# Optimization experiments

Hardware: AMD Instinct MI355X
Metric: run time of the kernel (lower is better)

The kernel has to match this reference:

```python
import jax, jax.numpy as jnp
import numpy as np

N_TOK, BATCH, D, MEM, H, W = 196, 64, 256, 2048, 16, 16


def setup_inputs() -> dict:
    key = jax.random.key(0)
    ks = jax.random.split(key, 9)
    w_scale = 1.0 / np.sqrt(D)  # ~ Linear default init scale
    return {
        "input_tokens": jax.random.normal(ks[0], (N_TOK, BATCH, D), jnp.float32),
        "ch_memory": jax.random.normal(ks[1], (MEM, D), jnp.float32) * 0.1,
        "ch_wq": jax.random.normal(ks[2], (D, D), jnp.float32) * w_scale,
        "ch_wk": jax.random.normal(ks[3], (D, D), jnp.float32) * w_scale,
        "ch_wv": jax.random.normal(ks[4], (D, D), jnp.float32) * w_scale,
        "sp_memory": jax.random.normal(ks[5], (MEM, H, W), jnp.float32) * 0.1,
        "sp_wq": jax.random.normal(ks[6], (D, D), jnp.float32) * w_scale,
        "sp_wk": jax.random.normal(ks[7], (D, D), jnp.float32) * w_scale,
        "sp_wv": jax.random.normal(ks[8], (D, D), jnp.float32) * w_scale,
    }


def reference(input_tokens, ch_memory, ch_wq, ch_wk, ch_wv,
              sp_memory, sp_wq, sp_wk, sp_wv):
    n_tok, batch, d = input_tokens.shape
    hw = d  # spatial branch requires feature_dim == H*W
    x = input_tokens.reshape(n_tok * batch, d)  # [NB, D]

    # ---- Channel memory branch: dot-product softmax read ----
    q = x @ ch_wq.T                       # [NB, D]
    k = ch_memory @ ch_wk.T               # [M, D]
    v = ch_memory @ ch_wv.T               # [M, D]
    scores = (q @ k.T) * (1.0 / jnp.sqrt(jnp.float32(d)))  # [NB, M]
    att_c = jax.nn.softmax(scores, axis=-1)
    out_c = att_c @ v                     # [NB, D]

    # ---- Spatial memory branch: SSIM-score softmax read ----
    mem_flat = sp_memory.reshape(sp_memory.shape[0], hw)  # [M, HW]
    qf = x @ sp_wq.T                      # [NB, HW]
    kf = mem_flat @ sp_wk.T               # [M, HW]
    vf = mem_flat @ sp_wv.T               # [M, HW]

    q_mean = jnp.mean(qf, axis=1, keepdims=True)          # [NB, 1]
    k_mean = jnp.mean(kf, axis=1, keepdims=True)          # [M, 1]
    q_var = jnp.var(qf, axis=1, ddof=1, keepdims=True)    # unbiased, like torch.var
    k_var = jnp.var(kf, axis=1, ddof=1, keepdims=True)
    cov = ((qf - q_mean) @ (kf - k_mean).T) / jnp.float32(hw - 1)  # [NB, M]

    c1, c2 = 0.01, 0.03
    mean_prod = q_mean @ k_mean.T                          # [NB, M]
    numerator = (2.0 * mean_prod + c1) * (2.0 * cov + c2)
    denominator = (q_mean ** 2 + (k_mean.T) ** 2 + c1) * (q_var + k_var.T + c2)
    ssim = numerator / (denominator + 1e-8)                # [NB, M]

    att_s = jax.nn.softmax(ssim, axis=-1)
    out_s = att_s @ vf                     # [NB, HW] == [NB, D]

    return (out_c + out_s).reshape(n_tok, batch, d)
```

## Files before the change

### kernel.cpp

```cpp
#include <hip/hip_runtime.h>

#define NBQ 12544
#define DM  256
#define MM  2048

typedef __attribute__((ext_vector_type(8)))  __bf16 bf16x8;
typedef __attribute__((ext_vector_type(4)))  float  floatx4;

__device__ __forceinline__ ushort f2bf(float x) {
    unsigned u = __float_as_uint(x);
    u += 0x7fffu + ((u >> 16) & 1u);
    return (ushort)(u >> 16);
}
__device__ __forceinline__ float bf2f(ushort h) {
    return __uint_as_float(((unsigned)h) << 16);
}
__device__ __forceinline__ ushort4 cvt4(float4 f) {
    union { __bf16 h[4]; ushort4 u; } r;
    r.h[0] = (__bf16)f.x; r.h[1] = (__bf16)f.y;
    r.h[2] = (__bf16)f.z; r.h[3] = (__bf16)f.w;
    return r.u;
}

__device__ __forceinline__ void glds16(const ushort* g, ushort* l) {
    __builtin_amdgcn_global_load_lds(
        (const __attribute__((address_space(1))) unsigned int*)g,
        (__attribute__((address_space(3))) unsigned int*)l, 16, 0, 0);
}

__global__ __launch_bounds__(256) void cvt_all_bf16(
    const float* __restrict__ x,   const float* __restrict__ ch_mem,
    const float* __restrict__ sp_mem,
    const float* __restrict__ cwq, const float* __restrict__ swq,
    const float* __restrict__ cwk, const float* __restrict__ cwv,
    const float* __restrict__ swk, const float* __restrict__ swv,
    ushort* __restrict__ xb, ushort* __restrict__ cmb,
    ushort* __restrict__ smb, ushort* __restrict__ wb)
{
    int bid = blockIdx.x;
    const float* src; ushort* dst; size_t off;
    if (bid < 392)      { src = x;      dst = xb;  off = (size_t)bid * 8192; }
    else if (bid < 456) { src = ch_mem; dst = cmb; off = (size_t)(bid - 392) * 8192; }
    else if (bid < 520) { src = sp_mem; dst = smb; off = (size_t)(bid - 456) * 8192; }
    else {
        int w = bid - 520, wi = w >> 3;
        if      (wi == 0) src = cwq;
        else if (wi == 1) src = swq;
        else if (wi == 2) src = cwk;
        else if (wi == 3) src = cwv;
        else if (wi == 4) src = swk;
        else              src = swv;
        dst = wb + (size_t)wi * 65536;
        off = (size_t)(w & 7) * 8192;
    }
    #pragma unroll
    for (int i = 0; i < 4; ++i) {
        size_t b = off + (size_t)i * 2048 + (size_t)threadIdx.x * 8;
        float4 a0 = *(const float4*)(src + b);
        float4 a1 = *(const float4*)(src + b + 4);
        *(ushort4*)(dst + b)     = cvt4(a0);
        *(ushort4*)(dst + b + 4) = cvt4(a1);
    }
}

#define PSTG(b, d0_)                                                          \
    { _Pragma("unroll") for (int p = 0; p < 2; ++p) {                         \
        int j = wv * 2 + p;                                                   \
        int R = j * 8 + (lane >> 3);                                          \
        int so = R * 256 + (d0_) + (((lane & 7) ^ (R & 7)) << 3);             \
        int doff = j * 512;                                                   \
        glds16(As_ + so, &SM[b][0][0][0] + doff);                             \
        glds16(W1_ + so, &SM[b][1][0][0] + doff);                             \
        glds16(W2_ + so, &SM[b][2][0][0] + doff);                             \
    } }

__global__ __launch_bounds__(256, 3) void gemm_proj_bf16(
    const ushort* __restrict__ xb,  const ushort* __restrict__ cmb,
    const ushort* __restrict__ smb, const ushort* __restrict__ wb,
    ushort* __restrict__ Qb,  ushort* __restrict__ QFb,
    ushort* __restrict__ Kb,  ushort* __restrict__ KFb,
    ushort* __restrict__ Vtb, ushort* __restrict__ VFtb)
{
    __shared__ ushort SM[2][3][64][64];

    int bid = blockIdx.x;
    const ushort* A; const ushort* W1; const ushort* W2;
    ushort* C1; ushort* C2; int nrows, trans2;
    if (bid < 784) {
        A = xb; W1 = wb; W2 = wb + 65536; C1 = Qb; C2 = QFb; nrows = NBQ; trans2 = 0;
    } else if (bid < 912) {
        A = cmb; W1 = wb + 2 * 65536; W2 = wb + 3 * 65536; C1 = Kb; C2 = Vtb;
        nrows = MM; trans2 = 1; bid -= 784;
    } else {
        A = smb; W1 = wb + 4 * 65536; W2 = wb + 5 * 65536; C1 = KFb; C2 = VFtb;
        nrows = MM; trans2 = 1; bid -= 912;
    }
    const int r0 = (bid >> 2) * 64;
    const int c0 = (bid & 3) * 64;

    const int tid  = threadIdx.x;
    const int wv   = tid >> 6;
    const int lane = tid & 63;
    const int quad = lane >> 4;
    const int l16  = lane & 15;
    const int rw = (wv & 1) * 32;
    const int cw = (wv >> 1) * 32;

    const ushort* As_ = A  + (size_t)r0 * 256;
    const ushort* W1_ = W1 + (size_t)c0 * 256;
    const ushort* W2_ = W2 + (size_t)c0 * 256;

    floatx4 acc1[2][2], acc2[2][2];
    #pragma unroll
    for (int i = 0; i < 2; ++i)
        #pragma unroll
        for (int j = 0; j < 2; ++j) {
            acc1[i][j] = (floatx4){0.f, 0.f, 0.f, 0.f};
            acc2[i][j] = (floatx4){0.f, 0.f, 0.f, 0.f};
        }

    PSTG(0, 0);
    __syncthreads();

    int buf = 0;
    const int kx = l16 & 7;
    for (int d0 = 0; d0 < 256; d0 += 64) {
        if (d0 + 64 < 256) PSTG(buf ^ 1, d0 + 64);
        #pragma unroll
        for (int kk = 0; kk < 64; kk += 32) {
            int off = (((kk >> 3) + quad) ^ kx) << 3;
            bf16x8 aA0 = *(const bf16x8*)&SM[buf][0][rw + l16][off];
            bf16x8 aA1 = *(const bf16x8*)&SM[buf][0][rw + 16 + l16][off];
            bf16x8 b10 = *(const bf16x8*)&SM[buf][1][cw + l16][off];
            bf16x8 b11 = *(const bf16x8*)&SM[buf][1][cw + 16 + l16][off];
            bf16x8 b20 = *(const bf16x8*)&SM[buf][2][cw + l16][off];
            bf16x8 b21 = *(const bf16x8*)&SM[buf][2][cw + 16 + l16][off];
            acc1[0][0] = __builtin_amdgcn_mfma_f32_16x16x32_bf16(aA0, b10, acc1[0][0], 0, 0, 0);
            acc1[0][1] = __builtin_amdgcn_mfma_f32_16x16x32_bf16(aA0, b11, acc1[0][1], 0, 0, 0);
            acc1[1][0] = __builtin_amdgcn_mfma_f32_16x16x32_bf16(aA1, b10, acc1[1][0], 0, 0, 0);
            acc1[1][1] = __builtin_amdgcn_mfma_f32_16x16x32_bf16(aA1, b11, acc1[1][1], 0, 0, 0);
            acc2[0][0] = __builtin_amdgcn_mfma_f32_16x16x32_bf16(aA0, b20, acc2[0][0], 0, 0, 0);
            acc2[0][1] = __builtin_amdgcn_mfma_f32_16x16x32_bf16(aA0, b21, acc2[0][1], 0, 0, 0);
            acc2[1][0] = __builtin_amdgcn_mfma_f32_16x16x32_bf16(aA1, b20, acc2[1][0], 0, 0, 0);
            acc2[1][1] = __builtin_amdgcn_mfma_f32_16x16x32_bf16(aA1, b21, acc2[1][1], 0, 0, 0);
        }
        __syncthreads();
        buf ^= 1;
    }

    #pragma unroll
    for (int ag = 0; ag < 2; ++ag)
        #pragma unroll
        for (int cg = 0; cg < 2; ++cg)
            #pragma unroll
            for (int i = 0; i < 4; ++i)
                C1[(size_t)(r0 + rw + ag * 16 + quad * 4 + i) * 256
                   + c0 + cw + cg * 16 + l16] = f2bf(acc1[ag][cg][i]);

    if (!trans2) {
        #pragma unroll
        for (int ag = 0; ag < 2; ++ag)
            #pragma unroll
            for (int cg = 0; cg < 2; ++cg)
                #pragma unroll
                for (int i = 0; i < 4; ++i)
                    C2[(size_t)(r0 + rw + ag * 16 + quad * 4 + i) * 256
                       + c0 + cw + cg * 16 + l16] = f2bf(acc2[ag][cg][i]);
    } else {
        __syncthreads();
        ushort (*W2s)[64] = SM[0][2];
        #pragma unroll
        for (int ag = 0; ag < 2; ++ag)
            #pragma unroll
            for (int cg = 0; cg < 2; ++cg)
                #pragma unroll
                for (int i = 0; i < 4; ++i) {
                    int col = rw + ag * 16 + quad * 4 + i;
                    int R   = cw + cg * 16 + l16;
                    W2s[R][(((col >> 3) ^ (R & 7)) << 3) + (col & 7)] =
                        f2bf(acc2[ag][cg][i]);
                }
        __syncthreads();
        const int col = tid >> 2;
        const int cj0 = (tid & 3) * 2;
        #pragma unroll
        for (int j = 0; j < 2; ++j) {
            int oc = cj0 + j;
            *(uint4*)(C2 + (size_t)(c0 + col) * nrows + r0 + oc * 8) =
                *(const uint4*)&W2s[col][(oc ^ (col & 7)) << 3];
        }
    }
}

__global__ __launch_bounds__(256) void gemm_proj_all(
    const float* __restrict__ x,      const float* __restrict__ ch_mem,
    const float* __restrict__ ch_wq,  const float* __restrict__ ch_wk,
    const float* __restrict__ ch_wv,  const float* __restrict__ sp_mem,
    const float* __restrict__ sp_wq,  const float* __restrict__ sp_wk,
    const float* __restrict__ sp_wv,
    ushort* __restrict__ Qb,  ushort* __restrict__ QFb,
    ushort* __restrict__ Kb,  ushort* __restrict__ KFb,
    ushort* __restrict__ Vtb, ushort* __restrict__ VFtb)
{
    __shared__ ushort As[64][72];
    __shared__ ushort W1s[64][72];
    __shared__ ushort W2s[64][72];

    int bid = blockIdx.x;
    const float* A; const float* W1; const float* W2;
    ushort* C1; ushort* C2; int nrows, trans2;
    if (bid < 784) {
        A = x; W1 = ch_wq; W2 = sp_wq; C1 = Qb; C2 = QFb; nrows = NBQ; trans2 = 0;
    } else if (bid < 912) {
        A = ch_mem; W1 = ch_wk; W2 = ch_wv; C1 = Kb; C2 = Vtb;
        nrows = MM; trans2 = 1; bid -= 784;
    } else {
        A = sp_mem; W1 = sp_wk; W2 = sp_wv; C1 = KFb; C2 = VFtb;
        nrows = MM; trans2 = 1; bid -= 912;
    }
    const int r0 = (bid >> 2) * 64;
    const int c0 = (bid & 3) * 64;

    const int tid  = threadIdx.x;
    const int wv   = tid >> 6;
    const int lane = tid & 63;
    const int quad = lane >> 4;
    const int l16  = lane & 15;
    const int rw = (wv & 1) * 32;
    const int cw = (wv >> 1) * 32;

    floatx4 acc1[2][2], acc2[2][2];
    #pragma unroll
    for (int i = 0; i < 2; ++i)
        #pragma unroll
        for (int j = 0; j < 2; ++j) {
            acc1[i][j] = (floatx4){0.f, 0.f, 0.f, 0.f};
            acc2[i][j] = (floatx4){0.f, 0.f, 0.f, 0.f};
        }

    float4 a4[4], w14[4], w24[4];
    #pragma unroll
    for (int it = 0; it < 4; ++it) {
        int idx = tid + it * 256;
        int r = idx >> 4, c4 = (idx & 15) * 4;
        a4[it]  = *(const float4*)(A  + (size_t)(r0 + r) * 256 + c4);
        w14[it] = *(const float4*)(W1 + (size_t)(c0 + r) * 256 + c4);
        w24[it] = *(const float4*)(W2 + (size_t)(c0 + r) * 256 + c4);
    }

    for (int d0 = 0; d0 < 256; d0 += 64) {
        __syncthreads();
        #pragma unroll
        for (int it = 0; it < 4; ++it) {
            int idx = tid + it * 256;
            int r = idx >> 4, c4 = (idx & 15) * 4;
            *(ushort4*)&As[r][c4]  = cvt4(a4[it]);
            *(ushort4*)&W1s[r][c4] = cvt4(w14[it]);
            *(ushort4*)&W2s[r][c4] = cvt4(w24[it]);
        }
        if (d0 + 64 < 256) {
            #pragma unroll
            for (int it = 0; it < 4; ++it) {
                int idx = tid + it * 256;
                int r = idx >> 4, c4 = (idx & 15) * 4;
                a4[it]  = *(const float4*)(A  + (size_t)(r0 + r) * 256 + d0 + 64 + c4);
                w14[it] = *(const float4*)(W1 + (size_t)(c0 + r) * 256 + d0 + 64 + c4);
                w24[it] = *(const float4*)(W2 + (size_t)(c0 + r) * 256 + d0 + 64 + c4);
            }
        }
        __syncthreads();
        #pragma unroll
        for (int kk = 0; kk < 64; kk += 32) {
            bf16x8 aA0 = *(const bf16x8*)&As[rw + l16][kk + quad * 8];
            bf16x8 aA1 = *(const bf16x8*)&As[rw + 16 + l16][kk + quad * 8];
            bf16x8 b10 = *(const bf16x8*)&W1s[cw + l16][kk + quad * 8];
            bf16x8 b11 = *(const bf16x8*)&W1s[cw + 16 + l16][kk + quad * 8];
            bf16x8 b20 = *(const bf16x8*)&W2s[cw + l16][kk + quad * 8];
            bf16x8 b21 = *(const bf16x8*)&W2s[cw + 16 + l16][kk + quad * 8];
            acc1[0][0] = __builtin_amdgcn_mfma_f32_16x16x32_bf16(aA0, b10, acc1[0][0], 0, 0, 0);
            acc1[0][1] = __builtin_amdgcn_mfma_f32_16x16x32_bf16(aA0, b11, acc1[0][1], 0, 0, 0);
            acc1[1][0] = __builtin_amdgcn_mfma_f32_16x16x32_bf16(aA1, b10, acc1[1][0], 0, 0, 0);
            acc1[1][1] = __builtin_amdgcn_mfma_f32_16x16x32_bf16(aA1, b11, acc1[1][1], 0, 0, 0);
            acc2[0][0] = __builtin_amdgcn_mfma_f32_16x16x32_bf16(aA0, b20, acc2[0][0], 0, 0, 0);
            acc2[0][1] = __builtin_amdgcn_mfma_f32_16x16x32_bf16(aA0, b21, acc2[0][1], 0, 0, 0);
            acc2[1][0] = __builtin_amdgcn_mfma_f32_16x16x32_bf16(aA1, b20, acc2[1][0], 0, 0, 0);
            acc2[1][1] = __builtin_amdgcn_mfma_f32_16x16x32_bf16(aA1, b21, acc2[1][1], 0, 0, 0);
        }
    }

    #pragma unroll
    for (int ag = 0; ag < 2; ++ag)
        #pragma unroll
        for (int cg = 0; cg < 2; ++cg)
            #pragma unroll
            for (int i = 0; i < 4; ++i)
                C1[(size_t)(r0 + rw + ag * 16 + quad * 4 + i) * 256
                   + c0 + cw + cg * 16 + l16] = f2bf(acc1[ag][cg][i]);

    if (!trans2) {
        #pragma unroll
        for (int ag = 0; ag < 2; ++ag)
            #pragma unroll
            for (int cg = 0; cg < 2; ++cg)
                #pragma unroll
                for (int i = 0; i < 4; ++i)
                    C2[(size_t)(r0 + rw + ag * 16 + quad * 4 + i) * 256
                       + c0 + cw + cg * 16 + l16] = f2bf(acc2[ag][cg][i]);
    } else {
        __syncthreads();
        #pragma unroll
        for (int ag = 0; ag < 2; ++ag)
            #pragma unroll
            for (int cg = 0; cg < 2; ++cg)
                #pragma unroll
                for (int i = 0; i < 4; ++i)
                    W2s[cw + cg * 16 + l16][rw + ag * 16 + quad * 4 + i] = f2bf(acc2[ag][cg][i]);
        __syncthreads();
        const int col = tid >> 2;
        const int seg = (tid & 3) * 16;
        #pragma unroll
        for (int j = 0; j < 2; ++j)
            *(uint4*)(C2 + (size_t)(c0 + col) * nrows + r0 + seg + j * 8) =
                *(const uint4*)&W2s[col][seg + j * 8];
    }
}

__global__ __launch_bounds__(256) void row_stats_kf(
    const ushort* __restrict__ KFb, float* __restrict__ km, float* __restrict__ kv)
{
    const int row  = blockIdx.x * 4 + (threadIdx.x >> 6);
    const int lane = threadIdx.x & 63;
    ushort4 u = *(const ushort4*)(KFb + (size_t)row * 256 + lane * 4);
    float a = bf2f(u.x), b = bf2f(u.y), c = bf2f(u.z), d = bf2f(u.w);
    float s  = a + b + c + d;
    float ss = a * a + b * b + c * c + d * d;
    #pragma unroll
    for (int off = 32; off > 0; off >>= 1) {
        s  += __shfl_down(s, off);
        ss += __shfl_down(ss, off);
    }
    if (lane == 0) {
        float m = s * (1.f / 256.f);
        km[row] = m;
        kv[row] = (ss - 256.f * m * m) * (1.f / 255.f) + 0.03f;
    }
}

#define STAGE_TILE(b, ti)                                                     \
    {                                                                         \
        const ushort* kp_ = kp0 + (size_t)(ti) * 32 * DM;                     \
        const ushort* vp_ = vp0 + (ti) * 32;                                  \
        ushort* dst_ = SMu + (b) * 16384;                                     \
        _Pragma("unroll")                                                     \
        for (int p = 0; p < 4; ++p) {                                         \
            int db = (wv * 4 + p) * 512;                                      \
            glds16(kp_ + offK[p], dst_ + db);                                 \
            glds16(vp_ + offV[p], dst_ + 8192 + db);                          \
        }                                                                     \
    }

template<int NHALF>
__global__ __launch_bounds__(256, 2) void fused_attn_1br(
    const ushort* __restrict__ Qb,  const ushort* __restrict__ QFb,
    const ushort* __restrict__ Kb,  const ushort* __restrict__ KFb,
    const ushort* __restrict__ Vtb, const ushort* __restrict__ VFtb,
    const float* __restrict__ km_, const float* __restrict__ kv_,
    float* __restrict__ part, float* __restrict__ denp)
{
    __shared__ ushort SMu[32768];

    const int tid  = threadIdx.x;
    const int wv   = tid >> 6;
    const int lane = tid & 63;
    const int quad = lane >> 4;
    const int l16  = lane & 15;

    const int NQC = NBQ / 128;
    const int per_br = NQC * NHALF;
    int bid = blockIdx.x;
    const int br  = (bid < per_br) ? 1 : 0;
    int rem = br ? bid : bid - per_br;
    const int half = rem / NQC;
    const int qc   = rem - half * NQC;
    const int q0   = qc * 128;
    const int kbase = half * (MM / NHALF);
    const int NT   = (MM / NHALF) / 32;

    const ushort* qsrc = br ? QFb : Qb;
    const ushort* Ksel = br ? KFb : Kb;
    const ushort* Vsel = br ? VFtb : Vtb;

    bf16x8 aQ0[8], aQ1[8];
    {
        const ushort* qp = qsrc + (size_t)(q0 + wv * 32 + l16) * DM + quad * 8;
        #pragma unroll
        for (int s = 0; s < 8; ++s) {
            aQ0[s] = *(const bf16x8*)(qp + s * 32);
            aQ1[s] = *(const bf16x8*)(qp + 16 * DM + s * 32);
        }
    }

    float qmv0 = 0.f, qvv0 = 0.f, qmv1 = 0.f, qvv1 = 0.f, qm20 = 0.f, qm21 = 0.f;
    if (br) {
        float s0 = 0.f, ss0 = 0.f, s1 = 0.f, ss1 = 0.f;
        #pragma unroll
        for (int s = 0; s < 8; ++s)
            #pragma unroll
            for (int j = 0; j < 8; ++j) {
                float v0 = (float)aQ0[s][j], v1 = (float)aQ1[s][j];
                s0 += v0; ss0 += v0 * v0; s1 += v1; ss1 += v1 * v1;
            }
        s0  += __shfl_xor(s0, 16, 64);  s0  += __shfl_xor(s0, 32, 64);
        ss0 += __shfl_xor(ss0, 16, 64); ss0 += __shfl_xor(ss0, 32, 64);
        s1  += __shfl_xor(s1, 16, 64);  s1  += __shfl_xor(s1, 32, 64);
        ss1 += __shfl_xor(ss1, 16, 64); ss1 += __shfl_xor(ss1, 32, 64);
        qmv0 = s0 * (1.f / 256.f);
        qvv0 = (ss0 - 256.f * qmv0 * qmv0) * (1.f / 255.f);
        qmv1 = s1 * (1.f / 256.f);
        qvv1 = (ss1 - 256.f * qmv1 * qmv1) * (1.f / 255.f);
        qm20 = qmv0 * qmv0 + 0.01f;
        qm21 = qmv1 * qmv1 + 0.01f;
    }

    int offK[4], offV[4];
    #pragma unroll
    for (int p = 0; p < 4; ++p) {
        int j  = wv * 4 + p;
        int Rk = 2 * j + (lane >> 5);
        int rk = (Rk & 3) + ((Rk >> 4) & 1) * 4 + ((Rk >> 2) & 3) * 8;
        int ck = (lane & 31) ^ (Rk & 7);
        offK[p] = rk * DM + ck * 8;
        int Rv = 16 * j + (lane >> 2);
        int cv = (lane & 3) ^ (Rv & 3);
        offV[p] = Rv * MM + cv * 8;
    }

    const ushort* kp0 = Ksel + (size_t)kbase * DM;
    const ushort* vp0 = Vsel + kbase;

    floatx4 acc0[16], acc1[16];
    #pragma unroll
    for (int t = 0; t < 16; ++t) {
        acc0[t] = (floatx4){0.f, 0.f, 0.f, 0.f};
        acc1[t] = (floatx4){0.f, 0.f, 0.f, 0.f};
    }
    float den0 = 0.f, den1 = 0.f;
    const int ksw  = l16 & 7;
    const int vswo = (quad ^ (l16 & 3)) * 8;

    STAGE_TILE(0, 0);
    __syncthreads();

    int buf = 0;
    for (int ti = 0; ti < NT; ++ti) {
        if (ti + 1 < NT) STAGE_TILE(buf ^ 1, ti + 1);

        const ushort* Ks = SMu + buf * 16384;
        const ushort* Vs = Ks + 8192;

        floatx4 S00 = (floatx4){0.f, 0.f, 0.f, 0.f};
        floatx4 S10 = (floatx4){0.f, 0.f, 0.f, 0.f};
        floatx4 S01 = (floatx4){0.f, 0.f, 0.f, 0.f};
        floatx4 S11 = (floatx4){0.f, 0.f, 0.f, 0.f};
        #pragma unroll
        for (int s = 0; s < 8; ++s) {
            int off = ((s * 4 + quad) ^ ksw) * 8;
            bf16x8 aK0 = *(const bf16x8*)(Ks + l16 * DM + off);
            bf16x8 aK1 = *(const bf16x8*)(Ks + 4096 + l16 * DM + off);
            S00 = __builtin_amdgcn_mfma_f32_16x16x32_bf16(aK0, aQ0[s], S00, 0, 0, 0);
            S10 = __builtin_amdgcn_mfma_f32_16x16x32_bf16(aK1, aQ0[s], S10, 0, 0, 0);
            S01 = __builtin_amdgcn_mfma_f32_16x16x32_bf16(aK0, aQ1[s], S01, 0, 0, 0);
            S11 = __builtin_amdgcn_mfma_f32_16x16x32_bf16(aK1, aQ1[s], S11, 0, 0, 0);
        }

        const int kk = kbase + ti * 32;
        float p0[8], p1[8];
        if (!br) {
            #pragma unroll
            for (int r = 0; r < 4; ++r) {
                p0[r]     = __expf(S00[r] * 0.0625f);
                p0[4 + r] = __expf(S10[r] * 0.0625f);
                p1[r]     = __expf(S01[r] * 0.0625f);
                p1[4 + r] = __expf(S11[r] * 0.0625f);
            }
        } else {
            floatx4 km0 = *(const floatx4*)(km_ + kk + 8 * quad);
            floatx4 km1 = *(const floatx4*)(km_ + kk + 8 * quad + 4);
            floatx4 kv0 = *(const floatx4*)(kv_ + kk + 8 * quad);
            floatx4 kv1 = *(const floatx4*)(kv_ + kk + 8 * quad + 4);
            #pragma unroll
            for (int r = 0; r < 4; ++r) {
                {
                    float kmr = km0[r];
                    float mp  = qmv0 * kmr;
                    float cov = (S00[r] - 256.f * mp) * (1.f / 255.f);
                    float num = (2.f * mp + 0.01f) * (2.f * cov + 0.03f);
                    float dn  = (qm20 + kmr * kmr) * (qvv0 + kv0[r]) + 1e-8f;
                    p0[r] = __expf(num / dn);
                }
                {
                    float kmr = km1[r];
                    float mp  = qmv0 * kmr;
                    float cov = (S10[r] - 256.f * mp) * (1.f / 255.f);
                    float num = (2.f * mp + 0.01f) * (2.f * cov + 0.03f);
                    float dn  = (qm20 + kmr * kmr) * (qvv0 + kv1[r]) + 1e-8f;
                    p0[4 + r] = __expf(num / dn);
                }
                {
                    float kmr = km0[r];
                    float mp  = qmv1 * kmr;
                    float cov = (S01[r] - 256.f * mp) * (1.f / 255.f);
                    float num = (2.f * mp + 0.01f) * (2.f * cov + 0.03f);
                    float dn  = (qm21 + kmr * kmr) * (qvv1 + kv0[r]) + 1e-8f;
                    p1[r] = __expf(num / dn);
                }
                {
                    float kmr = km1[r];
                    float mp  = qmv1 * kmr;
                    float cov = (S11[r] - 256.f * mp) * (1.f / 255.f);
                    float num = (2.f * mp + 0.01f) * (2.f * cov + 0.03f);
                    float dn  = (qm21 + kmr * kmr) * (qvv1 + kv1[r]) + 1e-8f;
                    p1[4 + r] = __expf(num / dn);
                }
            }
        }
        union { __bf16 h[8]; bf16x8 v; } ap0, ap1;
        #pragma unroll
        for (int j = 0; j < 8; ++j) {
            den0 += p0[j]; ap0.h[j] = (__bf16)p0[j];
            den1 += p1[j]; ap1.h[j] = (__bf16)p1[j];
        }

        #pragma unroll
        for (int t = 0; t < 16; ++t) {
            bf16x8 bV = *(const bf16x8*)(Vs + (t * 16 + l16) * 32 + vswo);
            acc0[t] = __builtin_amdgcn_mfma_f32_16x16x32_bf16(ap0.v, bV, acc0[t], 0, 0, 0);
            acc1[t] = __builtin_amdgcn_mfma_f32_16x16x32_bf16(ap1.v, bV, acc1[t], 0, 0, 0);
        }

        __syncthreads();
        buf ^= 1;
    }

    den0 += __shfl_xor(den0, 16, 64); den0 += __shfl_xor(den0, 32, 64);
    den1 += __shfl_xor(den1, 16, 64); den1 += __shfl_xor(den1, 32, 64);

    const int sec = br * NHALF + half;
    float* Np = part + (size_t)sec * ((size_t)NBQ * DM);
    #pragma unroll
    for (int t = 0; t < 16; ++t)
        #pragma unroll
        for (int r = 0; r < 4; ++r) {
            int row = q0 + wv * 32 + quad * 4 + r;
            Np[(size_t)row * DM + t * 16 + l16]        = acc0[t][r];
            Np[(size_t)(row + 16) * DM + t * 16 + l16] = acc1[t][r];
        }
    if (lane < 16) {
        denp[(size_t)sec * NBQ + q0 + wv * 32 + lane]      = den0;
        denp[(size_t)sec * NBQ + q0 + wv * 32 + 16 + lane] = den1;
    }
}

__global__ __launch_bounds__(256, 2) void fused_attn_fb(
    const ushort* __restrict__ Qb,  const ushort* __restrict__ QFb,
    const ushort* __restrict__ Kb,  const ushort* __restrict__ KFb,
    const ushort* __restrict__ Vtb, const ushort* __restrict__ VFtb,
    const float* __restrict__ km_, const float* __restrict__ kv_,
    float* __restrict__ out)
{
    __shared__ ushort SMu[32768];
    float* combuf = (float*)SMu;

    const int tid  = threadIdx.x;
    const int wv   = tid >> 6;
    const int lane = tid & 63;
    const int quad = lane >> 4;
    const int l16  = lane & 15;
    const int qsel = wv & 1;
    const int br   = wv >> 1;
    const int q0   = blockIdx.x * 32;

    const ushort* qsrc = br ? QFb : Qb;
    bf16x8 aQ[8];
    {
        const ushort* qp = qsrc + (size_t)(q0 + qsel * 16 + l16) * DM + quad * 8;
        #pragma unroll
        for (int s = 0; s < 8; ++s) aQ[s] = *(const bf16x8*)(qp + s * 32);
    }

    float qmv = 0.f, qvv = 0.f, qm2 = 0.f;
    if (br) {
        float sum = 0.f, ss = 0.f;
        #pragma unroll
        for (int s = 0; s < 8; ++s)
            #pragma unroll
            for (int jj = 0; jj < 8; ++jj) {
                float v = (float)aQ[s][jj];
                sum += v; ss += v * v;
            }
        sum += __shfl_xor(sum, 16, 64); sum += __shfl_xor(sum, 32, 64);
        ss  += __shfl_xor(ss, 16, 64);  ss  += __shfl_xor(ss, 32, 64);
        qmv = sum * (1.f / 256.f);
        qvv = (ss - 256.f * qmv * qmv) * (1.f / 255.f);
        qm2 = qmv * qmv + 0.01f;
    }

    int offK[4], offV[4];
    #pragma unroll
    for (int p = 0; p < 4; ++p) {
        int jw = wv * 4 + p;
        int Rk = 2 * jw + (lane >> 5);
        int rk = (Rk & 3) + ((Rk >> 4) & 1) * 4 + ((Rk >> 2) & 3) * 8;
        int ck = (lane & 31) ^ (Rk & 7);
        offK[p] = rk * DM + ck * 8;
        int Rv = 16 * jw + (lane >> 2);
        int cv = (lane & 3) ^ (Rv & 3);
        offV[p] = Rv * MM + cv * 8;
    }

    const ushort* kp  = Kb;
    const ushort* kfp = KFb;
    const ushort* vp  = Vtb;
    const ushort* vfp = VFtb;

    floatx4 acc[16];
    #pragma unroll
    for (int t = 0; t < 16; ++t) acc[t] = (floatx4){0.f, 0.f, 0.f, 0.f};
    float den = 0.f;

    const int ksw  = l16 & 7;
    const int vswo = (quad ^ (l16 & 3)) * 8;

    for (int kt = 0; kt < MM; kt += 32) {
        __syncthreads();
        #pragma unroll
        for (int p = 0; p < 4; ++p) {
            int db = (wv * 4 + p) * 512;
            glds16(kp  + offK[p], SMu + db);
            glds16(kfp + offK[p], SMu + 8192 + db);
            glds16(vp  + offV[p], SMu + 16384 + db);
            glds16(vfp + offV[p], SMu + 24576 + db);
        }
        kp += 32 * DM; kfp += 32 * DM; vp += 32; vfp += 32;
        __syncthreads();

        const ushort* Ks = SMu + (br ? 8192 : 0);
        floatx4 S0 = (floatx4){0.f, 0.f, 0.f, 0.f};
        floatx4 S1 = (floatx4){0.f, 0.f, 0.f, 0.f};
        #pragma unroll
        for (int s = 0; s < 8; ++s) {
            int off = ((s * 4 + quad) ^ ksw) * 8;
            bf16x8 aK0 = *(const bf16x8*)(Ks + l16 * DM + off);
            bf16x8 aK1 = *(const bf16x8*)(Ks + 4096 + l16 * DM + off);
            S0 = __builtin_amdgcn_mfma_f32_16x16x32_bf16(aK0, aQ[s], S0, 0, 0, 0);
            S1 = __builtin_amdgcn_mfma_f32_16x16x32_bf16(aK1, aQ[s], S1, 0, 0, 0);
        }

        float pb[8];
        if (!br) {
            #pragma unroll
            for (int r = 0; r < 4; ++r) {
                pb[r]     = __expf(S0[r] * 0.0625f);
                pb[4 + r] = __expf(S1[r] * 0.0625f);
            }
        } else {
            floatx4 km0 = *(const floatx4*)(km_ + kt + 8 * quad);
            floatx4 km1 = *(const floatx4*)(km_ + kt + 8 * quad + 4);
            floatx4 kv0 = *(const floatx4*)(kv_ + kt + 8 * quad);
            floatx4 kv1 = *(const floatx4*)(kv_ + kt + 8 * quad + 4);
            #pragma unroll
            for (int r = 0; r < 4; ++r) {
                {
                    float kmr = km0[r];
                    float mp  = qmv * kmr;
                    float cov = (S0[r] - 256.f * mp) * (1.f / 255.f);
                    float num = (2.f * mp + 0.01f) * (2.f * cov + 0.03f);
                    float dn  = (qm2 + kmr * kmr) * (qvv + kv0[r]) + 1e-8f;
                    pb[r] = __expf(num / dn);
                }
                {
                    float kmr = km1[r];
                    float mp  = qmv * kmr;
                    float cov = (S1[r] - 256.f * mp) * (1.f / 255.f);
                    float num = (2.f * mp + 0.01f) * (2.f * cov + 0.03f);
                    float dn  = (qm2 + kmr * kmr) * (qvv + kv1[r]) + 1e-8f;
                    pb[4 + r] = __expf(num / dn);
                }
            }
        }
        union { __bf16 h[8]; bf16x8 v; } ap;
        #pragma unroll
        for (int jj = 0; jj < 8; ++jj) {
            den += pb[jj];
            ap.h[jj] = (__bf16)pb[jj];
        }

        const ushort* Vs = SMu + (br ? 24576 : 16384);
        #pragma unroll
        for (int t = 0; t < 16; ++t) {
            bf16x8 bV = *(const bf16x8*)(Vs + (t * 16 + l16) * 32 + vswo);
            acc[t] = __builtin_amdgcn_mfma_f32_16x16x32_bf16(ap.v, bV, acc[t], 0, 0, 0);
        }
    }

    den += __shfl_xor(den, 16, 64);
    den += __shfl_xor(den, 32, 64);
    float rdn[4];
    #pragma unroll
    for (int r = 0; r < 4; ++r)
        rdn[r] = 1.f / __shfl(den, quad * 4 + r, 64);

    __syncthreads();
    if (br) {
        #pragma unroll
        for (int t = 0; t < 16; ++t)
            #pragma unroll
            for (int r = 0; r < 4; ++r)
                combuf[(qsel * 16 + quad * 4 + r) * 256 + t * 16 + l16] = acc[t][r] * rdn[r];
    }
    __syncthreads();
    if (!br) {
        #pragma unroll
        for (int t = 0; t < 16; ++t)
            #pragma unroll
            for (int r = 0; r < 4; ++r) {
                int ql = qsel * 16 + quad * 4 + r;
                out[(size_t)(q0 + ql) * DM + t * 16 + l16] =
                    acc[t][r] * rdn[r] + combuf[ql * 256 + t * 16 + l16];
            }
    }
}

__global__ __launch_bounds__(256) void combine_halves(
    const float* __restrict__ part, const float* __restrict__ denp,
    float* __restrict__ out)
{
    const size_t stride = (size_t)NBQ * 64;
    const floatx4* p4 = (const floatx4*)part;
    floatx4* o4 = (floatx4*)out;
    #pragma unroll
    for (int u = 0; u < 2; ++u) {
        size_t i = (size_t)blockIdx.x * 512 + (size_t)u * 256 + threadIdx.x;
        int q = (int)(i >> 6);
        float dc = 0.f, ds = 0.f;
        #pragma unroll
        for (int h = 0; h < 4; ++h) {
            dc += denp[(size_t)h * NBQ + q];
            ds += denp[(size_t)(4 + h) * NBQ + q];
        }
        float rc = 1.f / dc, rs = 1.f / ds;
        floatx4 nc = {0.f, 0.f, 0.f, 0.f}, ns = {0.f, 0.f, 0.f, 0.f};
        #pragma unroll
        for (int h = 0; h < 4; ++h) {
            nc += p4[(size_t)h * stride + i];
            ns += p4[(size_t)(4 + h) * stride + i];
        }
        o4[i] = nc * rc + ns * rs;
    }
}

extern "C" void kernel_launch(void* const* d_in, const int* in_sizes, int n_in,
                              void* d_out, int out_size, void* d_ws, size_t ws_size,
                              hipStream_t stream)
{
    const float* x      = (const float*)d_in[0];
    const float* ch_mem = (const float*)d_in[1];
    const float* ch_wq  = (const float*)d_in[2];
    const float* ch_wk  = (const float*)d_in[3];
    const float* ch_wv  = (const float*)d_in[4];
    const float* sp_mem = (const float*)d_in[5];
    const float* sp_wq  = (const float*)d_in[6];
    const float* sp_wk  = (const float*)d_in[7];
    const float* sp_wv  = (const float*)d_in[8];
    float* out = (float*)d_out;

    ushort* Qb   = (ushort*)d_ws;
    ushort* QFb  = Qb   + (size_t)NBQ * DM;
    ushort* Kb   = QFb  + (size_t)NBQ * DM;
    ushort* KFb  = Kb   + (size_t)MM * DM;
    ushort* Vtb  = KFb  + (size_t)MM * DM;
    ushort* VFtb = Vtb  + (size_t)MM * DM;
    float*  km   = (float*)(VFtb + (size_t)MM * DM);
    float*  kv   = km + MM;
    float*  denp = kv + MM;
    float*  part = denp + (size_t)8 * NBQ;

    ushort* xb   = (ushort*)part;
    ushort* cmb  = xb  + (size_t)NBQ * DM;
    ushort* smb  = cmb + (size_t)MM * DM;
    ushort* wb   = smb + (size_t)MM * DM;

    const size_t need = (size_t)((char*)(part + (size_t)8 * NBQ * DM) - (char*)d_ws);

    dim3 blk(256);
    if (ws_size >= need) {
        cvt_all_bf16<<<dim3(568), blk, 0, stream>>>(
            x, ch_mem, sp_mem, ch_wq, sp_wq, ch_wk, ch_wv, sp_wk, sp_wv,
            xb, cmb, smb, wb);
        gemm_proj_bf16<<<dim3(1040), blk, 0, stream>>>(
            xb, cmb, smb, wb, Qb, QFb, Kb, KFb, Vtb, VFtb);
        row_stats_kf<<<dim3(MM / 4), blk, 0, stream>>>(KFb, km, kv);
        fused_attn_1br<4><<<dim3(784), blk, 0, stream>>>(
            Qb, QFb, Kb, KFb, Vtb, VFtb, km, kv, part, denp);
        combine_halves<<<dim3(NBQ * DM / 4 / 512), blk, 0, stream>>>(part, denp, out);
    } else {
        gemm_proj_all<<<dim3(1040), blk, 0, stream>>>(
            x, ch_mem, ch_wq, ch_wk, ch_wv, sp_mem, sp_wq, sp_wk, sp_wv,
            Qb, QFb, Kb, KFb, Vtb, VFtb);
        row_stats_kf<<<dim3(MM / 4), blk, 0, stream>>>(KFb, km, kv);
        fused_attn_fb<<<dim3(NBQ / 32), blk, 0, stream>>>(
            Qb, QFb, Kb, KFb, Vtb, VFtb, km, kv, out);
    }
}
```

Measured before the change: 261.8 us.

## Fuse split-K combine into attention kernel via last-arriving-block counter

Removes the separate combine_halves launch. Each attention block now increments a per-query-chunk atomic counter after writing its partials. The last of the 8 blocks for that chunk sums the partial numerators and denominators and writes the output. This saves a kernel launch and lets the combine overlap with other blocks still running attention, at the cost of fences, atomics and a serial tail in the last block. The counters are reset in the conversion kernel.

```diff
diff --git a/kernel.cpp b/kernel.cpp
--- a/kernel.cpp
+++ b/kernel.cpp
@@ -35,9 +35,11 @@
     const float* __restrict__ cwk, const float* __restrict__ cwv,
     const float* __restrict__ swk, const float* __restrict__ swv,
     ushort* __restrict__ xb, ushort* __restrict__ cmb,
-    ushort* __restrict__ smb, ushort* __restrict__ wb)
+    ushort* __restrict__ smb, ushort* __restrict__ wb,
+    unsigned* __restrict__ cnt)
 {
     int bid = blockIdx.x;
+    if (bid == 0 && threadIdx.x < 128) cnt[threadIdx.x] = 0u;
     const float* src; ushort* dst; size_t off;
     if (bid < 392)      { src = x;      dst = xb;  off = (size_t)bid * 8192; }
     else if (bid < 456) { src = ch_mem; dst = cmb; off = (size_t)(bid - 392) * 8192; }
@@ -365,9 +367,11 @@
     const ushort* __restrict__ Kb,  const ushort* __restrict__ KFb,
     const ushort* __restrict__ Vtb, const ushort* __restrict__ VFtb,
     const float* __restrict__ km_, const float* __restrict__ kv_,
-    float* __restrict__ part, float* __restrict__ denp)
+    float* __restrict__ part, float* __restrict__ denp,
+    unsigned* __restrict__ cnt, float* __restrict__ out)
 {
     __shared__ ushort SMu[32768];
+    __shared__ unsigned arrv;
 
     const int tid  = threadIdx.x;
     const int wv   = tid >> 6;
@@ -559,6 +563,36 @@
         denp[(size_t)sec * NBQ + q0 + wv * 32 + lane]      = den0;
         denp[(size_t)sec * NBQ + q0 + wv * 32 + 16 + lane] = den1;
     }
+
+    __threadfence();
+    __syncthreads();
+    if (tid == 0) arrv = atomicAdd(&cnt[qc], 1u);
+    __syncthreads();
+    if (arrv == 2u * NHALF - 1u) {
+        __threadfence();
+        const size_t stride = (size_t)NBQ * 64;
+        const floatx4* p4 = (const floatx4*)part;
+        floatx4* o4 = (floatx4*)out;
+        #pragma unroll
+        for (int u = 0; u < 32; ++u) {
+            size_t i = (size_t)q0 * 64 + (size_t)u * 256 + tid;
+            int q = (int)(i >> 6);
+            float dc = 0.f, ds = 0.f;
+            #pragma unroll
+            for (int h = 0; h < NHALF; ++h) {
+                dc += denp[(size_t)h * NBQ + q];
+                ds += denp[(size_t)(NHALF + h) * NBQ + q];
+            }
+            float rc = 1.f / dc, rs = 1.f / ds;
+            floatx4 nc = {0.f, 0.f, 0.f, 0.f}, ns = {0.f, 0.f, 0.f, 0.f};
+            #pragma unroll
+            for (int h = 0; h < NHALF; ++h) {
+                nc += p4[(size_t)h * stride + i];
+                ns += p4[(size_t)(NHALF + h) * stride + i];
+            }
+            o4[i] = nc * rc + ns * rs;
+        }
+    }
 }
 
 __global__ __launch_bounds__(256, 2) void fused_attn_fb(
@@ -731,34 +765,6 @@
     }
 }
 
-__global__ __launch_bounds__(256) void combine_halves(
-    const float* __restrict__ part, const float* __restrict__ denp,
-    float* __restrict__ out)
-{
-    const size_t stride = (size_t)NBQ * 64;
-    const floatx4* p4 = (const floatx4*)part;
-    floatx4* o4 = (floatx4*)out;
-    #pragma unroll
-    for (int u = 0; u < 2; ++u) {
-        size_t i = (size_t)blockIdx.x * 512 + (size_t)u * 256 + threadIdx.x;
-        int q = (int)(i >> 6);
-        float dc = 0.f, ds = 0.f;
-        #pragma unroll
-        for (int h = 0; h < 4; ++h) {
-            dc += denp[(size_t)h * NBQ + q];
-            ds += denp[(size_t)(4 + h) * NBQ + q];
-        }
-        float rc = 1.f / dc, rs = 1.f / ds;
-        floatx4 nc = {0.f, 0.f, 0.f, 0.f}, ns = {0.f, 0.f, 0.f, 0.f};
-        #pragma unroll
-        for (int h = 0; h < 4; ++h) {
-            nc += p4[(size_t)h * stride + i];
-            ns += p4[(size_t)(4 + h) * stride + i];
-        }
-        o4[i] = nc * rc + ns * rs;
-    }
-}
-
 extern "C" void kernel_launch(void* const* d_in, const int* in_sizes, int n_in,
                               void* d_out, int out_size, void* d_ws, size_t ws_size,
                               hipStream_t stream)
@@ -783,7 +789,8 @@
     float*  km   = (float*)(VFtb + (size_t)MM * DM);
     float*  kv   = km + MM;
     float*  denp = kv + MM;
-    float*  part = denp + (size_t)8 * NBQ;
+    unsigned* cnt = (unsigned*)(denp + (size_t)8 * NBQ);
+    float*  part = (float*)(cnt + 128);
 
     ushort* xb   = (ushort*)part;
     ushort* cmb  = xb  + (size_t)NBQ * DM;
@@ -796,13 +803,12 @@
     if (ws_size >= need) {
         cvt_all_bf16<<<dim3(568), blk, 0, stream>>>(
             x, ch_mem, sp_mem, ch_wq, sp_wq, ch_wk, ch_wv, sp_wk, sp_wv,
-            xb, cmb, smb, wb);
+            xb, cmb, smb, wb, cnt);
         gemm_proj_bf16<<<dim3(1040), blk, 0, stream>>>(
             xb, cmb, smb, wb, Qb, QFb, Kb, KFb, Vtb, VFtb);
         row_stats_kf<<<dim3(MM / 4), blk, 0, stream>>>(KFb, km, kv);
         fused_attn_1br<4><<<dim3(784), blk, 0, stream>>>(
-            Qb, QFb, Kb, KFb, Vtb, VFtb, km, kv, part, denp);
-        combine_halves<<<dim3(NBQ * DM / 4 / 512), blk, 0, stream>>>(part, denp, out);
+            Qb, QFb, Kb, KFb, Vtb, VFtb, km, kv, part, denp, cnt, out);
     } else {
         gemm_proj_all<<<dim3(1040), blk, 0, stream>>>(
             x, ch_mem, ch_wq, ch_wk, ch_wv, sp_mem, sp_wq, sp_wk, sp_wv,
```

After: 363.1 us. 1.39x slower.
